# Optimization experiments

Hardware: AMD Instinct MI355X
Metric: run time of the kernel (lower is better)

The kernel has to match this reference:

```python
import jax, jax.numpy as jnp
import numpy as np

MAX_DISP = 24   # maxDisp = 192/8
K = 3           # box-filter kernel size
PAD = 1         # conv padding


def _cost_volume(inputs):
    # inputs: [B, 2c, H, W]; first half is input1, second half is input2
    b, c2, h, w = inputs.shape
    c = c2 // 2
    x1 = inputs[:, :c]
    x2 = inputs[:, c:]
    # pad input2 on the left by MAX_DISP (matches Fun.pad(..., (max_disp,0,0,0)))
    x2p = jnp.pad(x2, ((0, 0), (0, 0), (0, 0), (MAX_DISP, 0)))
    # original loop: d = MAX_DISP .. 0, slice [d:d+w]; output channel i uses
    # d = MAX_DISP - i, i.e. input2 shifted right by i pixels.
    slices = [
        jnp.einsum('bchw,bchw->bhw', x1,
                   x2p[:, :, :, MAX_DISP - i:MAX_DISP - i + w])
        for i in range(MAX_DISP + 1)
    ]
    corr = jnp.stack(slices, axis=1)  # [B, D+1, H, W]
    # per-channel (depthwise) conv with an all-ones KxK kernel == original
    # single-channel conv2d applied to each disparity slice
    ones = jnp.ones((MAX_DISP + 1, 1, K, K), dtype=inputs.dtype)
    out = jax.lax.conv_general_dilated(
        corr, ones,
        window_strides=(1, 1),
        padding=((PAD, PAD), (PAD, PAD)),
        feature_group_count=MAX_DISP + 1,
        dimension_numbers=('NCHW', 'OIHW', 'NCHW'))
    return out  # [B, MAX_DISP+1, H, W]


def setup_inputs() -> dict:
    key = jax.random.key(0)
    inputs = jax.random.normal(key, (16, 512, 64, 192), dtype=jnp.float32)
    return {"inputs": inputs}


def reference(inputs):
    return _cost_volume(inputs)
```

## Files before the change

kernel.cpp:

```cpp
#include <hip/hip_runtime.h>

constexpr int Bq = 16;
constexpr int Cc = 256;
constexpr int Hh = 64;
constexpr int Ww = 192;
constexpr int Dd = 25;
constexpr int HW = Hh * Ww;
constexpr int BSTRIDE = 2 * Cc * HW;
constexpr int CPR = 4;
constexpr int NR = Cc / CPR;
constexpr int ROWP = 24 + Ww;
constexpr int HT = 4;
constexpr int RT = HT + 2;
constexpr int TW = Ww + 4;
constexpr int NTHREADS = RT * 96;

__global__ __launch_bounds__(NTHREADS) void fused_kernel(const float* __restrict__ in,
                                                         float* __restrict__ out) {
  const int t  = threadIdx.x;
  const int r  = t / 96;
  const int u  = t % 96;
  const int w0 = 2 * u;

  const int lin  = blockIdx.x;
  const int slot = lin & 7;
  const int jj   = lin >> 3;
  const int b    = slot + 8 * (jj >> 4);
  const int tile = jj & 15;
  const int hbase = tile * HT;
  const int h = hbase + r - 1;
  const bool hvalid = (h >= 0) && (h < Hh);
  const int hc = hvalid ? h : 0;

  __shared__ float lds[RT * CPR * ROWP];
  auto x2s   = (float (*)[CPR][ROWP])lds;
  auto tilep = (float (*)[TW])lds;

  {
    const int rr  = t / (CPR * 24);
    const int rem = t % (CPR * 24);
    x2s[rr][rem / 24][rem % 24] = 0.0f;
  }

  const float* x1p = in + (size_t)b * BSTRIDE + (size_t)hc * Ww + w0;
  const float* x2p = x1p + (size_t)Cc * HW;

  float2 acc[Dd];
#pragma unroll
  for (int d = 0; d < Dd; ++d) acc[d] = make_float2(0.0f, 0.0f);

  float2 px1[CPR], px2[CPR];
#pragma unroll
  for (int c = 0; c < CPR; ++c) {
    if (hvalid) {
      px1[c] = *(const float2*)(x1p + c * HW);
      px2[c] = *(const float2*)(x2p + c * HW);
    } else {
      px1[c] = make_float2(0.0f, 0.0f);
      px2[c] = make_float2(0.0f, 0.0f);
    }
  }

  for (int rnd = 0; rnd < NR; ++rnd) {
    __syncthreads();
    float2 cx1[CPR];
#pragma unroll
    for (int c = 0; c < CPR; ++c) {
      cx1[c] = px1[c];
      *(float2*)&x2s[r][c][24 + w0] = px2[c];
    }
    __syncthreads();

    if (rnd + 1 < NR && hvalid) {
      const float* p1 = x1p + (size_t)(rnd + 1) * CPR * HW;
      const float* p2 = p1 + (size_t)Cc * HW;
#pragma unroll
      for (int c = 0; c < CPR; ++c) {
        px1[c] = *(const float2*)(p1 + c * HW);
        px2[c] = *(const float2*)(p2 + c * HW);
      }
    }

#pragma unroll
    for (int c = 0; c < CPR; ++c) {
      float win[26];
#pragma unroll
      for (int k = 0; k < 13; ++k) {
        const float2 v = *(const float2*)&x2s[r][c][w0 + 2 * k];
        win[2 * k]     = v.x;
        win[2 * k + 1] = v.y;
      }
      const float a0 = cx1[c].x, a1 = cx1[c].y;
#pragma unroll
      for (int d = 0; d < Dd; ++d) {
        acc[d].x = fmaf(a0, win[24 - d], acc[d].x);
        acc[d].y = fmaf(a1, win[25 - d], acc[d].y);
      }
    }
  }

  float* outb = out + (size_t)b * Dd * Hh * Ww;
#pragma unroll
  for (int d = 0; d < Dd; ++d) {
    __syncthreads();
    *(float2*)&tilep[r][2 + w0] = acc[d];
    if (u == 0)  { tilep[r][0]      = 0.0f; tilep[r][1]      = 0.0f; }
    if (u == 95) { tilep[r][TW - 2] = 0.0f; tilep[r][TW - 1] = 0.0f; }
    __syncthreads();
    if (r < HT) {
      float sx = 0.0f, sy = 0.0f;
#pragma unroll
      for (int q = 0; q < 3; ++q) {
        const float* trow = tilep[r + q];
        const float2 A = *(const float2*)&trow[w0];
        const float2 B = *(const float2*)&trow[w0 + 2];
        const float2 C = *(const float2*)&trow[w0 + 4];
        sx += A.y + B.x + B.y;
        sy += B.x + B.y + C.x;
      }
      *(float2*)(outb + ((size_t)d * Hh + hbase + r) * Ww + w0) = make_float2(sx, sy);
    }
  }
}

extern "C" void kernel_launch(void* const* d_in, const int* in_sizes, int n_in,
                              void* d_out, int out_size, void* d_ws, size_t ws_size,
                              hipStream_t stream) {
  const float* in = (const float*)d_in[0];
  float* out = (float*)d_out;
  (void)d_ws; (void)ws_size;

  fused_kernel<<<dim3(Bq * (Hh / HT)), dim3(NTHREADS), 0, stream>>>(in, out);
}
```

Before: 543.3 us.

## Split channel reduction across two thread halves with float4 register tiles

The channel reduction is split between two groups of 288 threads. Each group accumulates half of the channels into its own LDS buffer, and the partial sums are merged through LDS before the box filter runs. Each thread now handles four output columns held in float4 accumulators instead of two, which raises reuse of each loaded x2 window. x2 staging now uses cooperative float4 loads, and x1 is read directly each round with no prefetch. Costs are more registers (25 float4 accumulators), a larger LDS footprint, and an extra merge phase.

```diff
diff --git a/kernel.cpp b/kernel.cpp
--- a/kernel.cpp
+++ b/kernel.cpp
@@ -8,19 +8,21 @@
 constexpr int HW = Hh * Ww;
 constexpr int BSTRIDE = 2 * Cc * HW;
 constexpr int CPR = 4;
-constexpr int NR = Cc / CPR;
-constexpr int ROWP = 24 + Ww;
+constexpr int NR2 = (Cc / 2) / CPR;
 constexpr int HT = 4;
 constexpr int RT = HT + 2;
-constexpr int TW = Ww + 4;
-constexpr int NTHREADS = RT * 96;
+constexpr int ROWP = 24 + Ww;
+constexpr int TW = 200;
+constexpr int NTHREADS = 576;
 
-__global__ __launch_bounds__(NTHREADS) void fused_kernel(const float* __restrict__ in,
-                                                         float* __restrict__ out) {
+__global__ __launch_bounds__(NTHREADS, 3) void fused_kernel(const float* __restrict__ in,
+                                                            float* __restrict__ out) {
   const int t  = threadIdx.x;
-  const int r  = t / 96;
-  const int u  = t % 96;
-  const int w0 = 2 * u;
+  const int p  = t / 288;
+  const int s  = t % 288;
+  const int r  = s / 48;
+  const int u  = s % 48;
+  const int w0 = 4 * u;
 
   const int lin  = blockIdx.x;
   const int slot = lin & 7;
@@ -32,70 +34,109 @@
   const bool hvalid = (h >= 0) && (h < Hh);
   const int hc = hvalid ? h : 0;
 
-  __shared__ float lds[RT * CPR * ROWP];
-  auto x2s   = (float (*)[CPR][ROWP])lds;
+  __shared__ float lds[2 * RT * CPR * ROWP];
+  auto x2s   = (float (*)[RT][CPR][ROWP])lds;
+  auto mrg   = (float4 (*)[7])lds;
   auto tilep = (float (*)[TW])lds;
 
   {
-    const int rr  = t / (CPR * 24);
-    const int rem = t % (CPR * 24);
-    x2s[rr][rem / 24][rem % 24] = 0.0f;
+    const int pz  = t / 288;
+    const int g   = t % 288;
+    const int rz  = g / 48;
+    const int rem = g % 48;
+    const int cz  = rem / 12;
+    const int jz  = rem % 12;
+    *(float2*)&x2s[pz][rz][cz][2 * jz] = make_float2(0.0f, 0.0f);
   }
 
-  const float* x1p = in + (size_t)b * BSTRIDE + (size_t)hc * Ww + w0;
-  const float* x2p = x1p + (size_t)Cc * HW;
+  const float* gx2[4];
+  bool v2[4];
+  float* ldst[4];
+#pragma unroll
+  for (int k = 0; k < 4; ++k) {
+    const int lf = (k * 288 + s) * 4;
+    const int rk = lf / 768;
+    const int ck = (lf % 768) / 192;
+    const int wk = lf % 192;
+    const int hk = hbase + rk - 1;
+    v2[k] = (hk >= 0) && (hk < Hh);
+    const int hck = v2[k] ? hk : 0;
+    gx2[k]  = in + (size_t)b * BSTRIDE + (size_t)(Cc + 128 * p + ck) * HW
+                 + (size_t)hck * Ww + wk;
+    ldst[k] = &x2s[p][rk][ck][24 + wk];
+  }
 
-  float2 acc[Dd];
+  float4 acc[Dd];
 #pragma unroll
-  for (int d = 0; d < Dd; ++d) acc[d] = make_float2(0.0f, 0.0f);
+  for (int d = 0; d < Dd; ++d) acc[d] = make_float4(0.f, 0.f, 0.f, 0.f);
 
-  float2 px1[CPR], px2[CPR];
+  float4 px2[4];
 #pragma unroll
-  for (int c = 0; c < CPR; ++c) {
-    if (hvalid) {
-      px1[c] = *(const float2*)(x1p + c * HW);
-      px2[c] = *(const float2*)(x2p + c * HW);
-    } else {
-      px1[c] = make_float2(0.0f, 0.0f);
-      px2[c] = make_float2(0.0f, 0.0f);
+  for (int k = 0; k < 4; ++k)
+    px2[k] = v2[k] ? *(const float4*)gx2[k] : make_float4(0.f, 0.f, 0.f, 0.f);
+
+  const float* gx1 = in + (size_t)b * BSTRIDE + (size_t)(128 * p) * HW
+                        + (size_t)hc * Ww + w0;
+
+  for (int rnd = 0; rnd < NR2; ++rnd) {
+    __syncthreads();
+#pragma unroll
+    for (int k = 0; k < 4; ++k) *(float4*)ldst[k] = px2[k];
+    __syncthreads();
+
+    if (rnd + 1 < NR2) {
+#pragma unroll
+      for (int k = 0; k < 4; ++k) {
+        gx2[k] += (size_t)CPR * HW;
+        px2[k] = v2[k] ? *(const float4*)gx2[k] : make_float4(0.f, 0.f, 0.f, 0.f);
+      }
+    }
+
+    float4 cx1[CPR];
+#pragma unroll
+    for (int c = 0; c < CPR; ++c)
+      cx1[c] = hvalid ? *(const float4*)(gx1 + (size_t)(rnd * CPR + c) * HW)
+                      : make_float4(0.f, 0.f, 0.f, 0.f);
+
+#pragma unroll
+    for (int c = 0; c < CPR; ++c) {
+      const float4 cx = cx1[c];
+#pragma unroll
+      for (int k = 0; k < 7; ++k) {
+        const float4 wv = *(const float4*)&x2s[p][r][c][w0 + 4 * k];
+#pragma unroll
+        for (int e = 0; e < 4; ++e) {
+          const int j = 4 * k + e;
+          const float we = (e == 0) ? wv.x : (e == 1) ? wv.y : (e == 2) ? wv.z : wv.w;
+          const int d0_ = 24 - j;
+          if (d0_ >= 0 && d0_ <= 24)         acc[d0_].x     = fmaf(cx.x, we, acc[d0_].x);
+          if (d0_ + 1 >= 0 && d0_ + 1 <= 24) acc[d0_ + 1].y = fmaf(cx.y, we, acc[d0_ + 1].y);
+          if (d0_ + 2 >= 0 && d0_ + 2 <= 24) acc[d0_ + 2].z = fmaf(cx.z, we, acc[d0_ + 2].z);
+          if (d0_ + 3 >= 0 && d0_ + 3 <= 24) acc[d0_ + 3].w = fmaf(cx.w, we, acc[d0_ + 3].w);
+        }
+      }
     }
   }
 
-  for (int rnd = 0; rnd < NR; ++rnd) {
+#pragma unroll
+  for (int ch = 0; ch < 4; ++ch) {
+    const int d0 = ch * 7;
+    const int nd = (d0 + 7 <= Dd) ? 7 : (Dd - d0);
     __syncthreads();
-    float2 cx1[CPR];
+    if (p == 1) {
 #pragma unroll
-    for (int c = 0; c < CPR; ++c) {
-      cx1[c] = px1[c];
-      *(float2*)&x2s[r][c][24 + w0] = px2[c];
+      for (int j = 0; j < 7; ++j)
+        if (j < nd) mrg[s][j] = acc[d0 + j];
     }
     __syncthreads();
-
-    if (rnd + 1 < NR && hvalid) {
-      const float* p1 = x1p + (size_t)(rnd + 1) * CPR * HW;
-      const float* p2 = p1 + (size_t)Cc * HW;
+    if (p == 0) {
 #pragma unroll
-      for (int c = 0; c < CPR; ++c) {
-        px1[c] = *(const float2*)(p1 + c * HW);
-        px2[c] = *(const float2*)(p2 + c * HW);
-      }
-    }
-
-#pragma unroll
-    for (int c = 0; c < CPR; ++c) {
-      float win[26];
-#pragma unroll
-      for (int k = 0; k < 13; ++k) {
-        const float2 v = *(const float2*)&x2s[r][c][w0 + 2 * k];
-        win[2 * k]     = v.x;
-        win[2 * k + 1] = v.y;
-      }
-      const float a0 = cx1[c].x, a1 = cx1[c].y;
-#pragma unroll
-      for (int d = 0; d < Dd; ++d) {
-        acc[d].x = fmaf(a0, win[24 - d], acc[d].x);
-        acc[d].y = fmaf(a1, win[25 - d], acc[d].y);
-      }
+      for (int j = 0; j < 7; ++j)
+        if (j < nd) {
+          const float4 v = mrg[s][j];
+          acc[d0 + j].x += v.x; acc[d0 + j].y += v.y;
+          acc[d0 + j].z += v.z; acc[d0 + j].w += v.w;
+        }
     }
   }
 
@@ -103,22 +144,25 @@
 #pragma unroll
   for (int d = 0; d < Dd; ++d) {
     __syncthreads();
-    *(float2*)&tilep[r][2 + w0] = acc[d];
-    if (u == 0)  { tilep[r][0]      = 0.0f; tilep[r][1]      = 0.0f; }
-    if (u == 95) { tilep[r][TW - 2] = 0.0f; tilep[r][TW - 1] = 0.0f; }
+    if (p == 0) {
+      *(float4*)&tilep[r][2 + w0] = acc[d];
+      if (u == 0)  { tilep[r][0]   = 0.0f; tilep[r][1]   = 0.0f; }
+      if (u == 47) { tilep[r][194] = 0.0f; tilep[r][195] = 0.0f; }
+    }
     __syncthreads();
-    if (r < HT) {
-      float sx = 0.0f, sy = 0.0f;
+    if (p == 0 && r < HT) {
+      float s0 = 0.f, s1 = 0.f, s2 = 0.f, s3 = 0.f;
 #pragma unroll
       for (int q = 0; q < 3; ++q) {
-        const float* trow = tilep[r + q];
-        const float2 A = *(const float2*)&trow[w0];
-        const float2 B = *(const float2*)&trow[w0 + 2];
-        const float2 C = *(const float2*)&trow[w0 + 4];
-        sx += A.y + B.x + B.y;
-        sy += B.x + B.y + C.x;
+        const float4 L = *(const float4*)&tilep[r + q][w0];
+        const float4 R = *(const float4*)&tilep[r + q][w0 + 4];
+        s0 += L.y + L.z + L.w;
+        s1 += L.z + L.w + R.x;
+        s2 += L.w + R.x + R.y;
+        s3 += R.x + R.y + R.z;
       }
-      *(float2*)(outb + ((size_t)d * Hh + hbase + r) * Ww + w0) = make_float2(sx, sy);
+      *(float4*)(outb + ((size_t)d * Hh + hbase + r) * Ww + w0) =
+          make_float4(s0, s1, s2, s3);
     }
   }
 }
```

Result: slower. 622.7 us (+14.6%).
